# Kernel tuning notes

Hardware: AMD Instinct MI355X
Metric: run time of the kernel (lower is better)

Reference implementation:

```python
import jax, jax.numpy as jnp
import numpy as np
from jax import lax

B, W, K = 64, 128, 64      # batch, window_size, n_features
KS = 7                      # conv kernel size
EF = W                      # feature-attn embed dim (defaults to window_size, GATv1)
ET = 2 * K                  # temporal-attn embed dim (n_features doubled by GATv2)
H = 256                     # GRU hidden
FH = 256                    # forecast MLP hidden
ALPHA = 0.2                 # leaky relu slope


def _leaky(v):
    return jnp.where(v >= 0, v, ALPHA * v)


def setup_inputs() -> dict:
    key = jax.random.key(0)
    ks = jax.random.split(key, 20)
    s = 0.05
    inp = {
        "x": jax.random.normal(ks[0], (B, W, K), jnp.float32),
        # ConvLayer
        "conv_w": jax.random.normal(ks[1], (K, K, KS), jnp.float32) * s,
        "conv_b": jnp.zeros((K,), jnp.float32),
        # FeatureAttentionLayer (GATv1): lin W->EF, a:[2EF,1], bias [K,K]
        "feat_lin_w": jax.random.normal(ks[2], (EF, W), jnp.float32) * s,
        "feat_lin_b": jnp.zeros((EF,), jnp.float32),
        "feat_a": jax.random.normal(ks[3], (2 * EF, 1), jnp.float32) * s,
        "feat_bias": jnp.zeros((K, K), jnp.float32),
        # TemporalAttentionLayer (GATv2): lin 2K->ET, a:[ET,1], bias [W,W]
        "temp_lin_w": jax.random.normal(ks[4], (ET, 2 * K), jnp.float32) * s,
        "temp_lin_b": jnp.zeros((ET,), jnp.float32),
        "temp_a": jax.random.normal(ks[5], (ET, 1), jnp.float32) * s,
        "temp_bias": jnp.zeros((W, W), jnp.float32),
        # GRU (1 layer), input dim 3K
        "gru_wih": jax.random.normal(ks[6], (3 * H, 3 * K), jnp.float32) * s,
        "gru_whh": jax.random.normal(ks[7], (3 * H, H), jnp.float32) * s,
        "gru_bih": jnp.zeros((3 * H,), jnp.float32),
        "gru_bhh": jnp.zeros((3 * H,), jnp.float32),
        "fc0_w": jax.random.normal(ks[8], (FH, H), jnp.float32) * s,
        "fc0_b": jnp.zeros((FH,), jnp.float32),
        "fc1_w": jax.random.normal(ks[9], (FH, FH), jnp.float32) * s,
        "fc1_b": jnp.zeros((FH,), jnp.float32),
        "fc2_w": jax.random.normal(ks[10], (FH, FH), jnp.float32) * s,
        "fc2_b": jnp.zeros((FH,), jnp.float32),
        "fc3_w": jax.random.normal(ks[11], (K, FH), jnp.float32) * s,
        "fc3_b": jnp.zeros((K,), jnp.float32),
    }
    return inp


def _forward(x, conv_w, conv_b, feat_lin_w, feat_lin_b, feat_a, feat_bias,
             temp_lin_w, temp_lin_b, temp_a, temp_bias,
             gru_wih, gru_whh, gru_bih, gru_bhh,
             fc0_w, fc0_b, fc1_w, fc1_b, fc2_w, fc2_b, fc3_w, fc3_b):
    # --- ConvLayer: pad (k-1)//2 both sides, Conv1d K->K, ReLU ---
    pad = (KS - 1) // 2
    xc = x.transpose(0, 2, 1)                                   # [B,K,W]
    xc = jnp.pad(xc, ((0, 0), (0, 0), (pad, pad)))
    y = lax.conv_general_dilated(xc, conv_w, (1,), 'VALID',
                                 dimension_numbers=('NCH', 'OIH', 'NCH'))
    y = jax.nn.relu(y + conv_b[None, :, None]).transpose(0, 2, 1)  # [B,W,K]

    # --- FeatureAttentionLayer (GATv1): e_ij = leaky((Wx_i||Wx_j)·a) ---
    xf = y.transpose(0, 2, 1)                                   # [B,K,W]
    Wx = xf @ feat_lin_w.T + feat_lin_b                         # [B,K,EF]
    s1 = Wx @ feat_a[:EF, 0]                                    # [B,K]
    s2 = Wx @ feat_a[EF:, 0]                                    # [B,K]
    e_f = _leaky(s1[:, :, None] + s2[:, None, :]) + feat_bias   # [B,K,K]
    att_f = jax.nn.softmax(e_f, axis=2)
    h_feat = jax.nn.sigmoid(att_f @ xf).transpose(0, 2, 1)      # [B,W,K]

    # --- TemporalAttentionLayer (GATv2): g = leaky(lin(x_i||x_j)); e = g·a ---
    W1, W2 = temp_lin_w[:, :K], temp_lin_w[:, K:]               # split lin over concat halves
    p = y @ W1.T                                                # [B,W,ET]
    q = y @ W2.T                                                # [B,W,ET]
    g = _leaky(p[:, :, None, :] + q[:, None, :, :] + temp_lin_b)  # [B,W,W,ET]
    e_t = (g @ temp_a)[..., 0] + temp_bias                      # [B,W,W]
    att_t = jax.nn.softmax(e_t, axis=2)
    h_temp = jax.nn.sigmoid(att_t @ y)                          # [B,W,K]

    # --- concat + GRU over time ---
    z = jnp.concatenate([y, h_feat, h_temp], axis=2)            # [B,W,3K]

    def gru_step(h, xt):
        gi = xt @ gru_wih.T + gru_bih                           # [B,3H]
        gh = h @ gru_whh.T + gru_bhh
        ir, iz, inn = jnp.split(gi, 3, axis=1)
        hr, hz, hn = jnp.split(gh, 3, axis=1)
        r = jax.nn.sigmoid(ir + hr)
        zg = jax.nn.sigmoid(iz + hz)
        n = jnp.tanh(inn + r * hn)
        return (1.0 - zg) * n + zg * h, None

    h0 = jnp.zeros((z.shape[0], H), z.dtype)
    h_end, _ = lax.scan(gru_step, h0, z.transpose(1, 0, 2))     # [B,H]

    # --- Forecasting MLP (eval mode: dropout is identity) ---
    v = jax.nn.relu(h_end @ fc0_w.T + fc0_b)
    v = jax.nn.relu(v @ fc1_w.T + fc1_b)
    v = jax.nn.relu(v @ fc2_w.T + fc2_b)
    return v @ fc3_w.T + fc3_b                                  # [B,K]


def reference(x, conv_w, conv_b, feat_lin_w, feat_lin_b, feat_a, feat_bias,
              temp_lin_w, temp_lin_b, temp_a, temp_bias,
              gru_wih, gru_whh, gru_bih, gru_bhh,
              fc0_w, fc0_b, fc1_w, fc1_b, fc2_w, fc2_b, fc3_w, fc3_b):
    return _forward(x, conv_w, conv_b, feat_lin_w, feat_lin_b, feat_a, feat_bias,
                    temp_lin_w, temp_lin_b, temp_a, temp_bias,
                    gru_wih, gru_whh, gru_bih, gru_bhh,
                    fc0_w, fc0_b, fc1_w, fc1_b, fc2_w, fc2_b, fc3_w, fc3_b)
```

## Files before the change

### kernel.cpp

```cpp
#include <hip/hip_runtime.h>
#include <hip/hip_bf16.h>

typedef unsigned int uint;
typedef _Float16 half2_t __attribute__((ext_vector_type(2)));

union H2U { uint u; half2_t h; };

#if defined(__has_builtin)
#if __has_builtin(__builtin_amdgcn_fdot2)
#define HAVE_FDOT2 1
#endif
#endif

__device__ __forceinline__ float dot2acc(uint w, uint hh, float acc) {
    H2U a; a.u = w; H2U b; b.u = hh;
#ifdef HAVE_FDOT2
    return __builtin_amdgcn_fdot2(a.h, b.h, acc, false);
#else
    return acc + (float)a.h.x * (float)b.h.x + (float)a.h.y * (float)b.h.y;
#endif
}

#define OFF_Y    0u
#define OFF_Z    524288u
#define OFF_GI   2097152u
#define OFF_WHH  8388608u
#define OFF_C12  8486912u
#define OFF_DD   8487168u
#define OFF_HEND 8487424u

__global__ __launch_bounds__(256) void k_pack_prep(const float* __restrict__ whh, uint* __restrict__ w16,
                                                   const float* __restrict__ flw, const float* __restrict__ flb,
                                                   const float* __restrict__ fa, float* __restrict__ c12,
                                                   float* __restrict__ dd) {
    __shared__ float red[256];
    int bx = blockIdx.x, tid = threadIdx.x;
    if (bx < 384) {
        int idx = bx * 256 + tid;
        int tidq = idx / 192;
        int rem = idx - tidq * 192;
        int rp = rem >> 6;
        int i = rem & 63;
        int half = tidq >> 8;
        int mloc = tidq & 255;
        int row = 3 * mloc + rp;
        int pc = half * 64 + i;
        float a = whh[(size_t)row * 256 + 2 * pc];
        float b = whh[(size_t)row * 256 + 2 * pc + 1];
        H2U u; u.h.x = (_Float16)a; u.h.y = (_Float16)b;
        w16[idx] = u.u;
    } else {
        if (tid < 128) {
            float a = 0.f, b = 0.f;
            for (int e = 0; e < 128; ++e) {
                float w = flw[e * 128 + tid];
                a = fmaf(w, fa[e], a);
                b = fmaf(w, fa[128 + e], b);
            }
            c12[tid] = a;
            c12[128 + tid] = b;
        }
        int e = tid & 127;
        red[tid] = (tid < 128) ? flb[e] * fa[e] : flb[e] * fa[128 + e];
        __syncthreads();
        if (tid < 2) {
            float s = 0.f;
            for (int q = 0; q < 128; ++q) s += red[tid * 128 + q];
            dd[tid] = s;
        }
    }
}

__global__ __launch_bounds__(256) void k_conv(const float* __restrict__ x, const float* __restrict__ cw,
                                              const float* __restrict__ cb, float* __restrict__ y,
                                              float* __restrict__ z) {
    __shared__ float xT[64][41];
    __shared__ float cwL[64 * 64 * 7];
    int b = blockIdx.y, w0 = blockIdx.x * 32, tid = threadIdx.x;
    for (int idx = tid; idx < 38 * 64; idx += 256) {
        int wl = idx / 64, k = idx % 64;
        int wg = w0 - 3 + wl;
        xT[k][wl] = (wg >= 0 && wg < 128) ? x[((size_t)b * 128 + wg) * 64 + k] : 0.f;
    }
    for (int idx = tid; idx < 64 * 64 * 7; idx += 256) cwL[idx] = cw[idx];
    __syncthreads();
    int w_l = tid % 32, kog = tid / 32;
    float acc[8];
#pragma unroll
    for (int i = 0; i < 8; ++i) acc[i] = 0.f;
    for (int ki = 0; ki < 64; ++ki) {
        float x7[7];
#pragma unroll
        for (int u = 0; u < 7; ++u) x7[u] = xT[ki][w_l + u];
#pragma unroll
        for (int koi = 0; koi < 8; ++koi) {
            const float* wp = &cwL[((kog * 8 + koi) * 64 + ki) * 7];
#pragma unroll
            for (int u = 0; u < 7; ++u) acc[koi] = fmaf(x7[u], wp[u], acc[koi]);
        }
    }
    int w = w0 + w_l;
#pragma unroll
    for (int koi = 0; koi < 8; ++koi) {
        int ko = kog * 8 + koi;
        float v = acc[koi] + cb[ko];
        v = v > 0.f ? v : 0.f;
        y[((size_t)b * 128 + w) * 64 + ko] = v;
        z[((size_t)b * 128 + w) * 192 + ko] = v;
    }
}

__global__ __launch_bounds__(256) void k_feat(const float* __restrict__ y, const float* __restrict__ c12,
                                              const float* __restrict__ dd, const float* __restrict__ fb,
                                              float* __restrict__ z) {
    int b = blockIdx.y, w0 = blockIdx.x * 32, tid = threadIdx.x;
    __shared__ float s1L[64], s2L[64];
    __shared__ float attL[64][65];
    __shared__ float yL[32][64];
    __shared__ float cL[256];
    cL[tid] = c12[tid];
    for (int idx = tid; idx < 32 * 64; idx += 256) {
        int wl = idx / 64, j = idx % 64;
        yL[wl][j] = y[((size_t)b * 128 + w0 + wl) * 64 + j];
    }
    __syncthreads();
    if (tid < 128) {
        int k = tid % 64;
        const float* c = (tid < 64) ? cL : cL + 128;
        float acc = 0.f;
        for (int w = 0; w < 128; ++w) acc = fmaf(y[((size_t)b * 128 + w) * 64 + k], c[w], acc);
        if (tid < 64) s1L[k] = acc + dd[0]; else s2L[k] = acc + dd[1];
    }
    __syncthreads();
    if (tid < 64) {
        int k = tid;
        float s1 = s1L[k];
        float m = -1e30f;
        for (int j = 0; j < 64; ++j) {
            float v = s1 + s2L[j];
            float l = fmaxf(v, 0.2f * v);
            float e = l + fb[k * 64 + j];
            attL[k][j] = e;
            m = fmaxf(m, e);
        }
        float s = 0.f;
        for (int j = 0; j < 64; ++j) { float e = __expf(attL[k][j] - m); attL[k][j] = e; s += e; }
        float inv = 1.f / s;
        for (int j = 0; j < 64; ++j) attL[k][j] *= inv;
    }
    __syncthreads();
    int k_l = tid % 64, wg = tid / 64;
    for (int wi = 0; wi < 8; ++wi) {
        int wl = wg * 8 + wi;
        float acc = 0.f;
#pragma unroll 16
        for (int j = 0; j < 64; ++j) acc = fmaf(attL[k_l][j], yL[wl][j], acc);
        float hv = 1.f / (1.f + __expf(-acc));
        z[((size_t)b * 128 + w0 + wl) * 192 + 64 + k_l] = hv;
    }
}

__global__ __launch_bounds__(512) void k_temp(const float* __restrict__ y, const float* __restrict__ tlw,
                                              const float* __restrict__ tlb, const float* __restrict__ ta,
                                              const float* __restrict__ tbias, float* __restrict__ z) {
    int b = blockIdx.y, i0 = blockIdx.x * 32, tid = threadIdx.x;
    __shared__ __align__(16) float yT[64][132];
    __shared__ __align__(16) float qL[128][128];
    __shared__ __align__(16) float pL[32][128];
    __shared__ __align__(16) float etL[32][128];
    __shared__ __align__(16) float taL[128];
    __shared__ float mred[32][8], sred[32][8];
    __shared__ float mrow[32], invL[32];
    if (tid < 128) taL[tid] = ta[tid];
    for (int idx = tid; idx < 8192; idx += 512) {
        int j = idx >> 6, k = idx & 63;
        yT[k][j] = y[((size_t)b * 128 + j) * 64 + k];
    }
    __syncthreads();
    {
        int c = tid & 127, ih = tid >> 7;
        float w1r[64];
        const float4* w1p = (const float4*)(tlw + c * 128);
#pragma unroll
        for (int q4 = 0; q4 < 16; ++q4) {
            float4 v = w1p[q4];
            w1r[4 * q4] = v.x; w1r[4 * q4 + 1] = v.y; w1r[4 * q4 + 2] = v.z; w1r[4 * q4 + 3] = v.w;
        }
        float base = tlb[c];
#pragma unroll
        for (int ilb = 0; ilb < 2; ++ilb) {
            int j0 = i0 + ih * 8 + ilb * 4;
            float4 acc = {base, base, base, base};
            for (int k = 0; k < 64; ++k) {
                float4 yv = *((const float4*)&yT[k][j0]);
                float w = w1r[k];
                acc.x = fmaf(yv.x, w, acc.x); acc.y = fmaf(yv.y, w, acc.y);
                acc.z = fmaf(yv.z, w, acc.z); acc.w = fmaf(yv.w, w, acc.w);
            }
            int il = ih * 8 + ilb * 4;
            pL[il][c] = acc.x; pL[il + 1][c] = acc.y; pL[il + 2][c] = acc.z; pL[il + 3][c] = acc.w;
        }
    }
    {
        int j = tid & 127, ch = tid >> 7;
        float yreg[64];
#pragma unroll
        for (int k = 0; k < 64; ++k) yreg[k] = yT[k][j];
        for (int cc = 0; cc < 32; ++cc) {
            int c = __builtin_amdgcn_readfirstlane(ch * 32 + cc);
            const float* w2 = tlw + c * 128 + 64;
            float acc = 0.f;
#pragma unroll
            for (int k = 0; k < 64; ++k) acc = fmaf(yreg[k], w2[k], acc);
            qL[c][j] = acc;
        }
    }
    __syncthreads();
    {
        int jg = tid & 31, ih = tid >> 5;
        int j0 = jg * 4;
        int il0 = ih * 2;
        float4 acc0 = *((const float4*)(tbias + (size_t)(i0 + il0) * 128 + j0));
        float4 acc1 = *((const float4*)(tbias + (size_t)(i0 + il0 + 1) * 128 + j0));
        for (int c0 = 0; c0 < 128; c0 += 4) {
            float4 ta4 = *((const float4*)&taL[c0]);
            float4 p0 = *((const float4*)&pL[il0][c0]);
            float4 p1 = *((const float4*)&pL[il0 + 1][c0]);
            float4 q0 = *((const float4*)&qL[c0 + 0][j0]);
            float4 q1 = *((const float4*)&qL[c0 + 1][j0]);
            float4 q2 = *((const float4*)&qL[c0 + 2][j0]);
            float4 q3 = *((const float4*)&qL[c0 + 3][j0]);
#define ETSTEP(qv, tac, pa, pb) { \
            float u; \
            u = (pa) + qv.x; acc0.x = fmaf(fmaxf(u, 0.2f * u), (tac), acc0.x); \
            u = (pa) + qv.y; acc0.y = fmaf(fmaxf(u, 0.2f * u), (tac), acc0.y); \
            u = (pa) + qv.z; acc0.z = fmaf(fmaxf(u, 0.2f * u), (tac), acc0.z); \
            u = (pa) + qv.w; acc0.w = fmaf(fmaxf(u, 0.2f * u), (tac), acc0.w); \
            u = (pb) + qv.x; acc1.x = fmaf(fmaxf(u, 0.2f * u), (tac), acc1.x); \
            u = (pb) + qv.y; acc1.y = fmaf(fmaxf(u, 0.2f * u), (tac), acc1.y); \
            u = (pb) + qv.z; acc1.z = fmaf(fmaxf(u, 0.2f * u), (tac), acc1.z); \
            u = (pb) + qv.w; acc1.w = fmaf(fmaxf(u, 0.2f * u), (tac), acc1.w); }
            ETSTEP(q0, ta4.x, p0.x, p1.x)
            ETSTEP(q1, ta4.y, p0.y, p1.y)
            ETSTEP(q2, ta4.z, p0.z, p1.z)
            ETSTEP(q3, ta4.w, p0.w, p1.w)
#undef ETSTEP
        }
        *((float4*)&etL[il0][j0]) = acc0;
        *((float4*)&etL[il0 + 1][j0]) = acc1;
    }
    __syncthreads();
    if (tid < 256) {
        int il = tid >> 3, seg = tid & 7;
        const float4* ep = (const float4*)&etL[il][seg * 16];
        float m = -1e30f;
#pragma unroll
        for (int q = 0; q < 4; ++q) {
            float4 e = ep[q];
            m = fmaxf(m, fmaxf(fmaxf(e.x, e.y), fmaxf(e.z, e.w)));
        }
        mred[il][seg] = m;
    }
    __syncthreads();
    if (tid < 32) {
        float m = mred[tid][0];
#pragma unroll
        for (int s = 1; s < 8; ++s) m = fmaxf(m, mred[tid][s]);
        mrow[tid] = m;
    }
    __syncthreads();
    if (tid < 256) {
        int il = tid >> 3, seg = tid & 7;
        float m = mrow[il];
        float4* ep = (float4*)&etL[il][seg * 16];
        float s = 0.f;
#pragma unroll
        for (int q = 0; q < 4; ++q) {
            float4 e = ep[q];
            e.x = __expf(e.x - m); e.y = __expf(e.y - m);
            e.z = __expf(e.z - m); e.w = __expf(e.w - m);
            s += (e.x + e.y) + (e.z + e.w);
            ep[q] = e;
        }
        sred[il][seg] = s;
    }
    __syncthreads();
    if (tid < 32) {
        float s = 0.f;
#pragma unroll
        for (int q = 0; q < 8; ++q) s += sred[tid][q];
        invL[tid] = 1.f / s;
    }
    __syncthreads();
    {
        int k = tid & 63, ig = tid >> 6;
        float acc[4] = {0.f, 0.f, 0.f, 0.f};
        const float* yb = y + (size_t)b * 128 * 64 + k;
        for (int j0 = 0; j0 < 128; j0 += 4) {
            float yv[4];
#pragma unroll
            for (int jj = 0; jj < 4; ++jj) yv[jj] = yb[(size_t)(j0 + jj) * 64];
#pragma unroll
            for (int ii = 0; ii < 4; ++ii) {
                int il = ig * 4 + ii;
                float4 ev = *((const float4*)&etL[il][j0]);
                acc[ii] = fmaf(ev.x, yv[0], acc[ii]);
                acc[ii] = fmaf(ev.y, yv[1], acc[ii]);
                acc[ii] = fmaf(ev.z, yv[2], acc[ii]);
                acc[ii] = fmaf(ev.w, yv[3], acc[ii]);
            }
        }
#pragma unroll
        for (int ii = 0; ii < 4; ++ii) {
            int il = ig * 4 + ii;
            float hv = 1.f / (1.f + __expf(-acc[ii] * invL[il]));
            z[((size_t)b * 128 + i0 + il) * 192 + 128 + k] = hv;
        }
    }
}

__global__ __launch_bounds__(256) void k_gi(const float* __restrict__ z, const float* __restrict__ wih,
                                            const float* __restrict__ bih, float* __restrict__ gi) {
    int o0 = blockIdx.x * 128;
    int bt0 = blockIdx.y * 64;
    int tid = threadIdx.x;
    __shared__ __align__(16) float zL[64][68];
    __shared__ float wL[128][65];
    int ol = tid & 31;
    int r8 = (tid >> 5) * 8;
    float acc[8][4];
#pragma unroll
    for (int rr = 0; rr < 8; ++rr)
#pragma unroll
        for (int oo = 0; oo < 4; ++oo) acc[rr][oo] = 0.f;
    for (int mc = 0; mc < 3; ++mc) {
        int m0 = mc * 64;
        __syncthreads();
        {
            int mq = (tid & 15) * 4;
            int r = tid >> 4;
#pragma unroll
            for (int it = 0; it < 4; ++it, r += 16) {
                float4 v = *((const float4*)&z[(size_t)(bt0 + r) * 192 + m0 + mq]);
                *((float4*)&zL[r][mq]) = v;
            }
            int o = tid >> 4;
#pragma unroll
            for (int it = 0; it < 8; ++it, o += 16) {
                float4 v = *((const float4*)&wih[(size_t)(o0 + o) * 192 + m0 + mq]);
                wL[o][mq] = v.x; wL[o][mq + 1] = v.y; wL[o][mq + 2] = v.z; wL[o][mq + 3] = v.w;
            }
        }
        __syncthreads();
        for (int mb = 0; mb < 64; mb += 4) {
            float4 zv[8];
#pragma unroll
            for (int rr = 0; rr < 8; ++rr) zv[rr] = *((const float4*)&zL[r8 + rr][mb]);
#pragma unroll
            for (int mi = 0; mi < 4; ++mi) {
                float wv[4];
#pragma unroll
                for (int oo = 0; oo < 4; ++oo) wv[oo] = wL[ol + 32 * oo][mb + mi];
#pragma unroll
                for (int rr = 0; rr < 8; ++rr) {
                    float zc = (mi == 0) ? zv[rr].x : (mi == 1) ? zv[rr].y : (mi == 2) ? zv[rr].z : zv[rr].w;
#pragma unroll
                    for (int oo = 0; oo < 4; ++oo) acc[rr][oo] = fmaf(zc, wv[oo], acc[rr][oo]);
                }
            }
        }
    }
    float bo[4];
#pragma unroll
    for (int oo = 0; oo < 4; ++oo) bo[oo] = bih[o0 + ol + 32 * oo];
#pragma unroll
    for (int rr = 0; rr < 8; ++rr)
#pragma unroll
        for (int oo = 0; oo < 4; ++oo)
            gi[(size_t)(bt0 + r8 + rr) * 768 + o0 + ol + 32 * oo] = acc[rr][oo] + bo[oo];
}

#define KEEP4(W) asm volatile("" : "+v"(W.x), "+v"(W.y), "+v"(W.z), "+v"(W.w))
__global__ __launch_bounds__(512)
__attribute__((amdgpu_waves_per_eu(2, 2)))
void k_gru(const float* __restrict__ gi,
           const uint* __restrict__ w16,
           const float* __restrict__ bhh,
           float* __restrict__ hend) {
    int b = blockIdx.x, tid = threadIdx.x;
    int half = tid >> 8, mloc = tid & 255;
    int t = tid & 255;
    __shared__ __align__(16) uint4 hp4s[32];
    __shared__ float sH[2][768];
    const uint4* wp = (const uint4*)(w16 + (size_t)tid * 192);
    uint4 wa0 = wp[0],  wa1 = wp[1],  wa2 = wp[2],  wa3 = wp[3];
    uint4 wa4 = wp[4],  wa5 = wp[5],  wa6 = wp[6],  wa7 = wp[7];
    uint4 wa8 = wp[8],  wa9 = wp[9],  wa10 = wp[10], wa11 = wp[11];
    uint4 wa12 = wp[12], wa13 = wp[13], wa14 = wp[14], wa15 = wp[15];
    uint4 wb0 = wp[16], wb1 = wp[17], wb2 = wp[18], wb3 = wp[19];
    uint4 wb4 = wp[20], wb5 = wp[21], wb6 = wp[22], wb7 = wp[23];
    uint4 wb8 = wp[24], wb9 = wp[25], wb10 = wp[26], wb11 = wp[27];
    uint4 wb12 = wp[28], wb13 = wp[29], wb14 = wp[30], wb15 = wp[31];
    uint4 wc0 = wp[32], wc1 = wp[33], wc2 = wp[34], wc3 = wp[35];
    uint4 wc4 = wp[36], wc5 = wp[37], wc6 = wp[38], wc7 = wp[39];
    uint4 wc8 = wp[40], wc9 = wp[41], wc10 = wp[42], wc11 = wp[43];
    uint4 wc12 = wp[44], wc13 = wp[45], wc14 = wp[46], wc15 = wp[47];
    KEEP4(wa0); KEEP4(wa1); KEEP4(wa2); KEEP4(wa3);
    KEEP4(wa4); KEEP4(wa5); KEEP4(wa6); KEEP4(wa7);
    KEEP4(wa8); KEEP4(wa9); KEEP4(wa10); KEEP4(wa11);
    KEEP4(wa12); KEEP4(wa13); KEEP4(wa14); KEEP4(wa15);
    KEEP4(wb0); KEEP4(wb1); KEEP4(wb2); KEEP4(wb3);
    KEEP4(wb4); KEEP4(wb5); KEEP4(wb6); KEEP4(wb7);
    KEEP4(wb8); KEEP4(wb9); KEEP4(wb10); KEEP4(wb11);
    KEEP4(wb12); KEEP4(wb13); KEEP4(wb14); KEEP4(wb15);
    KEEP4(wc0); KEEP4(wc1); KEEP4(wc2); KEEP4(wc3);
    KEEP4(wc4); KEEP4(wc5); KEEP4(wc6); KEEP4(wc7);
    KEEP4(wc8); KEEP4(wc9); KEEP4(wc10); KEEP4(wc11);
    KEEP4(wc12); KEEP4(wc13); KEEP4(wc14); KEEP4(wc15);
    float br = 0.f, bz = 0.f, bn = 0.f;
    if (tid < 256) { br = bhh[t]; bz = bhh[256 + t]; bn = bhh[512 + t]; }
    float h = 0.f;
    if (tid < 32) { uint4 zz; zz.x = zz.y = zz.z = zz.w = 0u; hp4s[tid] = zz; }
    __syncthreads();
    const float* gib = gi + (size_t)b * 128 * 768;
    const uint4* hbase = hp4s + half * 16;
    int m3 = 3 * mloc;
    for (int s = 0; s < 128; ++s) {
        float gr = 0.f, gz = 0.f, gn = 0.f;
        if (tid < 256) {
            gr = gib[s * 768 + t];
            gz = gib[s * 768 + 256 + t];
            gn = gib[s * 768 + 512 + t];
        }
        float a0 = 0.f, a1 = 0.f, b0 = 0.f, b1 = 0.f, c0 = 0.f, c1 = 0.f;
#define GSTEP(J, WA, WB, WC) { uint4 hv = hbase[J]; \
        a0 = dot2acc(WA.x, hv.x, a0); a1 = dot2acc(WA.y, hv.y, a1); \
        a0 = dot2acc(WA.z, hv.z, a0); a1 = dot2acc(WA.w, hv.w, a1); \
        b0 = dot2acc(WB.x, hv.x, b0); b1 = dot2acc(WB.y, hv.y, b1); \
        b0 = dot2acc(WB.z, hv.z, b0); b1 = dot2acc(WB.w, hv.w, b1); \
        c0 = dot2acc(WC.x, hv.x, c0); c1 = dot2acc(WC.y, hv.y, c1); \
        c0 = dot2acc(WC.z, hv.z, c0); c1 = dot2acc(WC.w, hv.w, c1); }
        GSTEP(0, wa0, wb0, wc0)   GSTEP(1, wa1, wb1, wc1)
        GSTEP(2, wa2, wb2, wc2)   GSTEP(3, wa3, wb3, wc3)
        GSTEP(4, wa4, wb4, wc4)   GSTEP(5, wa5, wb5, wc5)
        GSTEP(6, wa6, wb6, wc6)   GSTEP(7, wa7, wb7, wc7)
        GSTEP(8, wa8, wb8, wc8)   GSTEP(9, wa9, wb9, wc9)
        GSTEP(10, wa10, wb10, wc10) GSTEP(11, wa11, wb11, wc11)
        GSTEP(12, wa12, wb12, wc12) GSTEP(13, wa13, wb13, wc13)
        GSTEP(14, wa14, wb14, wc14) GSTEP(15, wa15, wb15, wc15)
#undef GSTEP
        sH[half][m3 + 0] = a0 + a1;
        sH[half][m3 + 1] = b0 + b1;
        sH[half][m3 + 2] = c0 + c1;
        __syncthreads();
        if (tid < 256) {
            float hr = sH[0][t] + sH[1][t] + br;
            float hz = sH[0][256 + t] + sH[1][256 + t] + bz;
            float hn = sH[0][512 + t] + sH[1][512 + t] + bn;
            float r  = 1.f / (1.f + __expf(-(gr + hr)));
            float zg = 1.f / (1.f + __expf(-(gz + hz)));
            float nx = gn + r * hn;
            float n  = 1.f - 2.f / (1.f + __expf(2.f * nx));
            h = (1.f - zg) * n + zg * h;
            ((_Float16*)hp4s)[t] = (_Float16)h;
        }
        __syncthreads();
    }
    if (tid < 256) hend[b * 256 + t] = h;
}

__global__ __launch_bounds__(256) void k_fc(const float* __restrict__ hend,
                                            const float* __restrict__ w0, const float* __restrict__ b0,
                                            const float* __restrict__ w1, const float* __restrict__ b1,
                                            const float* __restrict__ w2, const float* __restrict__ b2,
                                            const float* __restrict__ w3, const float* __restrict__ b3,
                                            float* __restrict__ out) {
    int b = blockIdx.x, tid = threadIdx.x;
    __shared__ float bufA[256], bufB[256];
    bufA[tid] = hend[b * 256 + tid];
    __syncthreads();
    {
        float acc = b0[tid];
        const float* wrow = &w0[tid * 256];
#pragma unroll 8
        for (int m = 0; m < 256; ++m) acc = fmaf(wrow[m], bufA[m], acc);
        bufB[tid] = fmaxf(acc, 0.f);
    }
    __syncthreads();
    {
        float acc = b1[tid];
        const float* wrow = &w1[tid * 256];
#pragma unroll 8
        for (int m = 0; m < 256; ++m) acc = fmaf(wrow[m], bufB[m], acc);
        bufA[tid] = fmaxf(acc, 0.f);
    }
    __syncthreads();
    {
        float acc = b2[tid];
        const float* wrow = &w2[tid * 256];
#pragma unroll 8
        for (int m = 0; m < 256; ++m) acc = fmaf(wrow[m], bufA[m], acc);
        bufB[tid] = fmaxf(acc, 0.f);
    }
    __syncthreads();
    if (tid < 64) {
        float acc = b3[tid];
        const float* wrow = &w3[tid * 256];
#pragma unroll 8
        for (int m = 0; m < 256; ++m) acc = fmaf(wrow[m], bufB[m], acc);
        out[b * 64 + tid] = acc;
    }
}

extern "C" void kernel_launch(void* const* d_in, const int* in_sizes, int n_in,
                              void* d_out, int out_size, void* d_ws, size_t ws_size,
                              hipStream_t stream) {
    const float* x    = (const float*)d_in[0];
    const float* cw   = (const float*)d_in[1];
    const float* cb   = (const float*)d_in[2];
    const float* flw  = (const float*)d_in[3];
    const float* flb  = (const float*)d_in[4];
    const float* fa   = (const float*)d_in[5];
    const float* fb   = (const float*)d_in[6];
    const float* tlw  = (const float*)d_in[7];
    const float* tlb  = (const float*)d_in[8];
    const float* ta   = (const float*)d_in[9];
    const float* tb   = (const float*)d_in[10];
    const float* wih  = (const float*)d_in[11];
    const float* whh  = (const float*)d_in[12];
    const float* bih  = (const float*)d_in[13];
    const float* bhh  = (const float*)d_in[14];
    const float* fc0w = (const float*)d_in[15];
    const float* fc0b = (const float*)d_in[16];
    const float* fc1w = (const float*)d_in[17];
    const float* fc1b = (const float*)d_in[18];
    const float* fc2w = (const float*)d_in[19];
    const float* fc2b = (const float*)d_in[20];
    const float* fc3w = (const float*)d_in[21];
    const float* fc3b = (const float*)d_in[22];

    float* wsf  = (float*)d_ws;
    float* y    = wsf + OFF_Y;
    float* z    = wsf + OFF_Z;
    float* gi   = wsf + OFF_GI;
    uint*  w16  = (uint*)(wsf + OFF_WHH);
    float* c12  = wsf + OFF_C12;
    float* dd   = wsf + OFF_DD;
    float* hend = wsf + OFF_HEND;
    float* out  = (float*)d_out;

    k_pack_prep<<<385, 256, 0, stream>>>(whh, w16, flw, flb, fa, c12, dd);
    k_conv<<<dim3(4, 64), 256, 0, stream>>>(x, cw, cb, y, z);
    k_feat<<<dim3(4, 64), 256, 0, stream>>>(y, c12, dd, fb, z);
    k_temp<<<dim3(4, 64), 512, 0, stream>>>(y, tlw, tlb, ta, tb, z);
    k_gi<<<dim3(6, 128), 256, 0, stream>>>(z, wih, bih, gi);
    k_gru<<<64, 512, 0, stream>>>(gi, w16, bhh, hend);
    k_fc<<<64, 256, 0, stream>>>(hend, fc0w, fc0b, fc1w, fc1b, fc2w, fc2b, fc3w, fc3b, out);
}
```

Measured before the change: 417.6 us.

## Split GRU recurrent matvec across four thread quarters per block

The GRU kernel now uses 1024 threads per block instead of 512. Each thread holds a quarter of the hidden-dimension slice of W_hh in registers (24 uint4 instead of 48), and the weight packing is re-laid out to match. This halves the serial dot-product chain per step and frees registers to allow 4 waves per EU. In exchange, each step reduces four partial sums through a larger shared buffer, and barriers now cover twice as many waves.

```diff
diff --git a/kernel.cpp b/kernel.cpp
--- a/kernel.cpp
+++ b/kernel.cpp
@@ -37,14 +37,14 @@
     int bx = blockIdx.x, tid = threadIdx.x;
     if (bx < 384) {
         int idx = bx * 256 + tid;
-        int tidq = idx / 192;
-        int rem = idx - tidq * 192;
-        int rp = rem >> 6;
-        int i = rem & 63;
-        int half = tidq >> 8;
+        int tidq = idx / 96;
+        int rem = idx - tidq * 96;
+        int rp = rem >> 5;
+        int i = rem & 31;
+        int quarter = tidq >> 8;
         int mloc = tidq & 255;
         int row = 3 * mloc + rp;
-        int pc = half * 64 + i;
+        int pc = quarter * 32 + i;
         float a = whh[(size_t)row * 256 + 2 * pc];
         float b = whh[(size_t)row * 256 + 2 * pc + 1];
         H2U u; u.h.x = (_Float16)a; u.h.y = (_Float16)b;
@@ -381,49 +381,32 @@
 }
 
 #define KEEP4(W) asm volatile("" : "+v"(W.x), "+v"(W.y), "+v"(W.z), "+v"(W.w))
-__global__ __launch_bounds__(512)
-__attribute__((amdgpu_waves_per_eu(2, 2)))
+__global__ __launch_bounds__(1024)
+__attribute__((amdgpu_waves_per_eu(4, 4)))
 void k_gru(const float* __restrict__ gi,
            const uint* __restrict__ w16,
            const float* __restrict__ bhh,
            float* __restrict__ hend) {
     int b = blockIdx.x, tid = threadIdx.x;
-    int half = tid >> 8, mloc = tid & 255;
+    int quarter = tid >> 8, mloc = tid & 255;
     int t = tid & 255;
     __shared__ __align__(16) uint4 hp4s[32];
-    __shared__ float sH[2][768];
-    const uint4* wp = (const uint4*)(w16 + (size_t)tid * 192);
-    uint4 wa0 = wp[0],  wa1 = wp[1],  wa2 = wp[2],  wa3 = wp[3];
-    uint4 wa4 = wp[4],  wa5 = wp[5],  wa6 = wp[6],  wa7 = wp[7];
-    uint4 wa8 = wp[8],  wa9 = wp[9],  wa10 = wp[10], wa11 = wp[11];
-    uint4 wa12 = wp[12], wa13 = wp[13], wa14 = wp[14], wa15 = wp[15];
-    uint4 wb0 = wp[16], wb1 = wp[17], wb2 = wp[18], wb3 = wp[19];
-    uint4 wb4 = wp[20], wb5 = wp[21], wb6 = wp[22], wb7 = wp[23];
-    uint4 wb8 = wp[24], wb9 = wp[25], wb10 = wp[26], wb11 = wp[27];
-    uint4 wb12 = wp[28], wb13 = wp[29], wb14 = wp[30], wb15 = wp[31];
-    uint4 wc0 = wp[32], wc1 = wp[33], wc2 = wp[34], wc3 = wp[35];
-    uint4 wc4 = wp[36], wc5 = wp[37], wc6 = wp[38], wc7 = wp[39];
-    uint4 wc8 = wp[40], wc9 = wp[41], wc10 = wp[42], wc11 = wp[43];
-    uint4 wc12 = wp[44], wc13 = wp[45], wc14 = wp[46], wc15 = wp[47];
-    KEEP4(wa0); KEEP4(wa1); KEEP4(wa2); KEEP4(wa3);
-    KEEP4(wa4); KEEP4(wa5); KEEP4(wa6); KEEP4(wa7);
-    KEEP4(wa8); KEEP4(wa9); KEEP4(wa10); KEEP4(wa11);
-    KEEP4(wa12); KEEP4(wa13); KEEP4(wa14); KEEP4(wa15);
-    KEEP4(wb0); KEEP4(wb1); KEEP4(wb2); KEEP4(wb3);
-    KEEP4(wb4); KEEP4(wb5); KEEP4(wb6); KEEP4(wb7);
-    KEEP4(wb8); KEEP4(wb9); KEEP4(wb10); KEEP4(wb11);
-    KEEP4(wb12); KEEP4(wb13); KEEP4(wb14); KEEP4(wb15);
-    KEEP4(wc0); KEEP4(wc1); KEEP4(wc2); KEEP4(wc3);
-    KEEP4(wc4); KEEP4(wc5); KEEP4(wc6); KEEP4(wc7);
-    KEEP4(wc8); KEEP4(wc9); KEEP4(wc10); KEEP4(wc11);
-    KEEP4(wc12); KEEP4(wc13); KEEP4(wc14); KEEP4(wc15);
+    __shared__ float sH[4][768];
+    uint4 wv[24];
+    {
+        const uint4* wp = (const uint4*)(w16 + (size_t)tid * 96);
+#pragma unroll
+        for (int i = 0; i < 24; ++i) wv[i] = wp[i];
+#pragma unroll
+        for (int i = 0; i < 24; ++i) KEEP4(wv[i]);
+    }
     float br = 0.f, bz = 0.f, bn = 0.f;
     if (tid < 256) { br = bhh[t]; bz = bhh[256 + t]; bn = bhh[512 + t]; }
     float h = 0.f;
     if (tid < 32) { uint4 zz; zz.x = zz.y = zz.z = zz.w = 0u; hp4s[tid] = zz; }
     __syncthreads();
     const float* gib = gi + (size_t)b * 128 * 768;
-    const uint4* hbase = hp4s + half * 16;
+    const uint4* hbase = hp4s + quarter * 8;
     int m3 = 3 * mloc;
     for (int s = 0; s < 128; ++s) {
         float gr = 0.f, gz = 0.f, gn = 0.f;
@@ -433,30 +416,27 @@
             gn = gib[s * 768 + 512 + t];
         }
         float a0 = 0.f, a1 = 0.f, b0 = 0.f, b1 = 0.f, c0 = 0.f, c1 = 0.f;
-#define GSTEP(J, WA, WB, WC) { uint4 hv = hbase[J]; \
-        a0 = dot2acc(WA.x, hv.x, a0); a1 = dot2acc(WA.y, hv.y, a1); \
-        a0 = dot2acc(WA.z, hv.z, a0); a1 = dot2acc(WA.w, hv.w, a1); \
-        b0 = dot2acc(WB.x, hv.x, b0); b1 = dot2acc(WB.y, hv.y, b1); \
-        b0 = dot2acc(WB.z, hv.z, b0); b1 = dot2acc(WB.w, hv.w, b1); \
-        c0 = dot2acc(WC.x, hv.x, c0); c1 = dot2acc(WC.y, hv.y, c1); \
-        c0 = dot2acc(WC.z, hv.z, c0); c1 = dot2acc(WC.w, hv.w, c1); }
-        GSTEP(0, wa0, wb0, wc0)   GSTEP(1, wa1, wb1, wc1)
-        GSTEP(2, wa2, wb2, wc2)   GSTEP(3, wa3, wb3, wc3)
-        GSTEP(4, wa4, wb4, wc4)   GSTEP(5, wa5, wb5, wc5)
-        GSTEP(6, wa6, wb6, wc6)   GSTEP(7, wa7, wb7, wc7)
-        GSTEP(8, wa8, wb8, wc8)   GSTEP(9, wa9, wb9, wc9)
-        GSTEP(10, wa10, wb10, wc10) GSTEP(11, wa11, wb11, wc11)
-        GSTEP(12, wa12, wb12, wc12) GSTEP(13, wa13, wb13, wc13)
-        GSTEP(14, wa14, wb14, wc14) GSTEP(15, wa15, wb15, wc15)
-#undef GSTEP
-        sH[half][m3 + 0] = a0 + a1;
-        sH[half][m3 + 1] = b0 + b1;
-        sH[half][m3 + 2] = c0 + c1;
+#pragma unroll
+        for (int j = 0; j < 8; ++j) {
+            uint4 hv = hbase[j];
+            uint4 wa = wv[j];
+            uint4 wb = wv[8 + j];
+            uint4 wc = wv[16 + j];
+            a0 = dot2acc(wa.x, hv.x, a0); a1 = dot2acc(wa.y, hv.y, a1);
+            a0 = dot2acc(wa.z, hv.z, a0); a1 = dot2acc(wa.w, hv.w, a1);
+            b0 = dot2acc(wb.x, hv.x, b0); b1 = dot2acc(wb.y, hv.y, b1);
+            b0 = dot2acc(wb.z, hv.z, b0); b1 = dot2acc(wb.w, hv.w, b1);
+            c0 = dot2acc(wc.x, hv.x, c0); c1 = dot2acc(wc.y, hv.y, c1);
+            c0 = dot2acc(wc.z, hv.z, c0); c1 = dot2acc(wc.w, hv.w, c1);
+        }
+        sH[quarter][m3 + 0] = a0 + a1;
+        sH[quarter][m3 + 1] = b0 + b1;
+        sH[quarter][m3 + 2] = c0 + c1;
         __syncthreads();
         if (tid < 256) {
-            float hr = sH[0][t] + sH[1][t] + br;
-            float hz = sH[0][256 + t] + sH[1][256 + t] + bz;
-            float hn = sH[0][512 + t] + sH[1][512 + t] + bn;
+            float hr = ((sH[0][t] + sH[1][t]) + (sH[2][t] + sH[3][t])) + br;
+            float hz = ((sH[0][256 + t] + sH[1][256 + t]) + (sH[2][256 + t] + sH[3][256 + t])) + bz;
+            float hn = ((sH[0][512 + t] + sH[1][512 + t]) + (sH[2][512 + t] + sH[3][512 + t])) + bn;
             float r  = 1.f / (1.f + __expf(-(gr + hr)));
             float zg = 1.f / (1.f + __expf(-(gz + hz)));
             float nx = gn + r * hn;
@@ -554,6 +534,6 @@
     k_feat<<<dim3(4, 64), 256, 0, stream>>>(y, c12, dd, fb, z);
     k_temp<<<dim3(4, 64), 512, 0, stream>>>(y, tlw, tlb, ta, tb, z);
     k_gi<<<dim3(6, 128), 256, 0, stream>>>(z, wih, bih, gi);
-    k_gru<<<64, 512, 0, stream>>>(gi, w16, bhh, hend);
+    k_gru<<<64, 1024, 0, stream>>>(gi, w16, bhh, hend);
     k_fc<<<64, 256, 0, stream>>>(hend, fc0w, fc0b, fc1w, fc1b, fc2w, fc2b, fc3w, fc3b, out);
 }
```

Result: faster. 407.8 us (-2.3%).
